# Performance work log

Hardware: AMD Instinct MI355X
Metric: run time of the kernel (lower is better)

Reference implementation:

```python
import jax, jax.numpy as jnp
import numpy as np

N_FEATURES = 1024
N_OUTPUTS = 512
N = 32768
N_DECISIONS = 3  # root + 2 internal nodes (depth-2 tree)
N_LEAVES = 4


def setup_inputs() -> dict:
    key = jax.random.key(0)
    k_x, k_dw, k_db, k_lw, k_lb = jax.random.split(key, 5)
    xs = jax.random.normal(k_x, (N, N_FEATURES), dtype=jnp.float32)
    # decision hyperplanes for nodes [root, left-child, right-child]
    dec_w = jax.random.normal(k_dw, (N_DECISIONS, N_FEATURES), dtype=jnp.float32) / np.sqrt(N_FEATURES)
    dec_b = jax.random.normal(k_db, (N_DECISIONS,), dtype=jnp.float32) * 0.01
    # linear leaves, ordered [LL, LR, RL, RR]
    leaf_w = jax.random.normal(k_lw, (N_LEAVES, N_FEATURES, N_OUTPUTS), dtype=jnp.float32) / np.sqrt(N_FEATURES)
    leaf_b = jax.random.normal(k_lb, (N_LEAVES, N_OUTPUTS), dtype=jnp.float32) * 0.01
    return {"xs": xs, "dec_w": dec_w, "dec_b": dec_b, "leaf_w": leaf_w, "leaf_b": leaf_b}


def reference(xs, dec_w, dec_b, leaf_w, leaf_b):
    # decisions at all 3 branch nodes: [N, 3] boolean (True -> go right)
    d = (xs @ dec_w.T + dec_b) > 0
    d0, d1, d2 = d[:, 0], d[:, 1], d[:, 2]
    # leaf index per sample: root False -> left subtree (node 1), True -> right subtree (node 2)
    leaf_idx = jnp.where(
        d0,
        jnp.where(d2, 3, 2),
        jnp.where(d1, 1, 0),
    )  # [N]
    # compute all leaf outputs densely (equivalent math to masked dispatch), then select
    outs = jnp.einsum("nf,kfd->nkd", xs, leaf_w) + leaf_b  # [N, 4, D]
    out = jnp.take_along_axis(outs, leaf_idx[:, None, None], axis=1)[:, 0]  # [N, D]
    return out
```

## Files before the change

kernel.cpp:

```cpp
#include <hip/hip_runtime.h>
#include <hip/hip_bf16.h>
#include <stdint.h>

#define NROWS 32768
#define NFEAT 1024
#define NOUT  512

typedef __attribute__((ext_vector_type(8))) short bf16x8;
typedef __attribute__((ext_vector_type(4))) float f32x4;

#define WS_CNT  0
#define WS_LIST 256
#define WS_BT   524544
#define WS_XB   (WS_BT + (size_t)4 * NOUT * NFEAT * 2)
#define WS_NEEDED (WS_XB + (size_t)NROWS * NFEAT * 2)

#define NDEC_BLOCKS 1024
#define NTR_BLOCKS  512

__global__ __launch_bounds__(64) void zero_cnt_kernel(int* __restrict__ cnt) {
  if (threadIdx.x < 4) cnt[threadIdx.x] = 0;
}

__global__ __launch_bounds__(256) void decide_tr_kernel(
    const float* __restrict__ xs, const float* __restrict__ dw,
    const float* __restrict__ db, const float* __restrict__ lw,
    __hip_bfloat16* __restrict__ bt, int* __restrict__ cnt,
    int* __restrict__ list, __hip_bfloat16* __restrict__ xsb ) {
  __shared__ float smem[32 * 33];
  const int tid = threadIdx.x;
  int b = blockIdx.x;

  if (b >= NDEC_BLOCKS) {
    int tb = b - NDEC_BLOCKS;
    int l = tb >> 7;
    int t = tb & 127;
    int d0 = (t >> 3) * 32;
    int k00 = (t & 7) * 128;
    int x = tid & 31, y = tid >> 5;
    const float* src = lw + (size_t)l * NFEAT * NOUT;
    __hip_bfloat16* dst = bt + (size_t)l * NOUT * NFEAT;
    float (*tile)[33] = (float(*)[33])smem;
    for (int kk = 0; kk < 4; ++kk) {
      int k0 = k00 + kk * 32;
#pragma unroll
      for (int i = 0; i < 4; ++i)
        tile[y * 4 + i][x] = src[(size_t)(k0 + y * 4 + i) * NOUT + d0 + x];
      __syncthreads();
#pragma unroll
      for (int i = 0; i < 4; ++i)
        dst[(size_t)(d0 + y * 4 + i) * NFEAT + k0 + x] =
            __float2bfloat16(tile[x][y * 4 + i]);
      __syncthreads();
    }
    return;
  }

  int* leaf_of = (int*)smem;
  const int lane = tid & 63;
  const int wv = tid >> 6;

  f32x4 w0[4], w1[4], w2[4];
#pragma unroll
  for (int c = 0; c < 2; ++c)
#pragma unroll
    for (int h = 0; h < 2; ++h) {
      int idx = c * 512 + lane * 8 + h * 4;
      w0[c * 2 + h] = *(const f32x4*)(dw + idx);
      w1[c * 2 + h] = *(const f32x4*)(dw + NFEAT + idx);
      w2[c * 2 + h] = *(const f32x4*)(dw + 2 * NFEAT + idx);
    }
  float b0 = db[0], b1 = db[1], b2 = db[2];

  int rowbase = b * 32 + wv * 8;
  for (int r = 0; r < 8; ++r) {
    int row = rowbase + r;
    const float* xr = xs + (size_t)row * NFEAT;
    float s0 = 0.f, s1 = 0.f, s2 = 0.f;
#pragma unroll
    for (int c = 0; c < 2; ++c) {
      int idx = c * 512 + lane * 8;
      f32x4 xv0 = *(const f32x4*)(xr + idx);
      f32x4 xv1 = *(const f32x4*)(xr + idx + 4);
#pragma unroll
      for (int j = 0; j < 4; ++j) {
        s0 += xv0[j] * w0[c * 2][j] + xv1[j] * w0[c * 2 + 1][j];
        s1 += xv0[j] * w1[c * 2][j] + xv1[j] * w1[c * 2 + 1][j];
        s2 += xv0[j] * w2[c * 2][j] + xv1[j] * w2[c * 2 + 1][j];
      }
      if (xsb) {
        union { bf16x8 v; __hip_bfloat16 h[8]; } pk;
#pragma unroll
        for (int j = 0; j < 4; ++j) {
          pk.h[j] = __float2bfloat16(xv0[j]);
          pk.h[j + 4] = __float2bfloat16(xv1[j]);
        }
        *(bf16x8*)(xsb + (size_t)row * NFEAT + idx) = pk.v;
      }
    }
#pragma unroll
    for (int off = 32; off > 0; off >>= 1) {
      s0 += __shfl_xor(s0, off);
      s1 += __shfl_xor(s1, off);
      s2 += __shfl_xor(s2, off);
    }
    if (lane == 0) {
      int lf = (s0 + b0 > 0.f) ? ((s2 + b2 > 0.f) ? 3 : 2)
                               : ((s1 + b1 > 0.f) ? 1 : 0);
      leaf_of[wv * 8 + r] = lf;
    }
  }
  __syncthreads();

  if (tid < 64) {
    int i = tid;
    int myleaf = (i < 32) ? leaf_of[i] : -1;
    int myrow = b * 32 + i;
    unsigned long long m0 = __ballot(myleaf == 0);
    unsigned long long m1 = __ballot(myleaf == 1);
    unsigned long long m2 = __ballot(myleaf == 2);
    unsigned long long m3 = __ballot(myleaf == 3);
    unsigned long long mym = (myleaf == 0) ? m0 : (myleaf == 1) ? m1
                           : (myleaf == 2) ? m2 : (myleaf == 3) ? m3 : 0ull;
    unsigned long long below = (1ull << i) - 1ull;
    int rank = __popcll(mym & below);
    int base = 0;
    if (i < 4) {
      unsigned long long mi = (i == 0) ? m0 : (i == 1) ? m1 : (i == 2) ? m2 : m3;
      base = atomicAdd(&cnt[i], __popcll(mi));
    }
    int mybase = __shfl(base, (myleaf < 0) ? 0 : myleaf);
    if (i < 32) list[myleaf * NROWS + mybase + rank] = myrow;
  }
}

#define BM 128
#define BN 128
#define BK 64
#define KSTEPS (NFEAT / BK)

__device__ __forceinline__ bool decode_tile(const int* cnt, int& leaf, int& mloc,
                                            int& ntile, int& cc) {
  int bid = blockIdx.x;
  int cpx = (int)(gridDim.x >> 3);
  int swz = (bid & 7) * cpx + (bid >> 3);
  int mtile = swz >> 2;
  ntile = swz & 3;
  int c0 = cnt[0], c1 = cnt[1], c2 = cnt[2], c3 = cnt[3];
  int t0 = (c0 + BM - 1) / BM, t1 = (c1 + BM - 1) / BM;
  int t2 = (c2 + BM - 1) / BM, t3 = (c3 + BM - 1) / BM;
  if (mtile < t0)                     { leaf = 0; mloc = mtile;                cc = c0; }
  else if (mtile < t0 + t1)           { leaf = 1; mloc = mtile - t0;           cc = c1; }
  else if (mtile < t0 + t1 + t2)      { leaf = 2; mloc = mtile - t0 - t1;      cc = c2; }
  else if (mtile < t0 + t1 + t2 + t3) { leaf = 3; mloc = mtile - t0 - t1 - t2; cc = c3; }
  else return false;
  return true;
}

__global__ __launch_bounds__(256) void gemm_lds_kernel(
    const __hip_bfloat16* __restrict__ xsb, const __hip_bfloat16* __restrict__ bt,
    const float* __restrict__ lb, const int* __restrict__ cnt,
    const int* __restrict__ list, float* __restrict__ out) {
  __shared__ __hip_bfloat16 Al[BM * BK];
  __shared__ __hip_bfloat16 Bl[BN * BK];
  __shared__ int rows_s[BM];

  int leaf, mloc, ntile, cc;
  if (!decode_tile(cnt, leaf, mloc, ntile, cc)) return;

  const int tid = threadIdx.x;
  if (tid < BM) {
    int i = mloc * BM + tid;
    rows_s[tid] = (i < cc) ? list[leaf * NROWS + i] : -1;
  }
  __syncthreads();

  const int lane = tid & 63;
  const int wv = tid >> 6;
  const int g8 = (((lane & 7) ^ (lane >> 3)) << 3);
  const __hip_bfloat16* asrc[4];
  const __hip_bfloat16* bsrc[4];
#pragma unroll
  for (int j = 0; j < 4; ++j) {
    int tr = wv * 32 + j * 8 + (lane >> 3);
    int grow = rows_s[tr];
    if (grow < 0) grow = 0;
    asrc[j] = xsb + (size_t)grow * NFEAT + g8;
    bsrc[j] = bt + ((size_t)leaf * NOUT + ntile * BN + tr) * NFEAT + g8;
  }

  const int wr = (wv >> 1) * 64;
  const int wc = (wv & 1) * 64;
  f32x4 acc[4][4];
#pragma unroll
  for (int m = 0; m < 4; ++m)
#pragma unroll
    for (int n = 0; n < 4; ++n) acc[m][n] = (f32x4){0.f, 0.f, 0.f, 0.f};

  for (int ks = 0; ks < KSTEPS; ++ks) {
    if (ks) __syncthreads();
#pragma unroll
    for (int j = 0; j < 4; ++j) {
      __builtin_amdgcn_global_load_lds(
          (const __attribute__((address_space(1))) void*)(asrc[j] + ks * BK),
          (__attribute__((address_space(3))) void*)(&Al[(wv * 4 + j) * 512]),
          16, 0, 0);
      __builtin_amdgcn_global_load_lds(
          (const __attribute__((address_space(1))) void*)(bsrc[j] + ks * BK),
          (__attribute__((address_space(3))) void*)(&Bl[(wv * 4 + j) * 512]),
          16, 0, 0);
    }
    __syncthreads();

#pragma unroll
    for (int kk = 0; kk < 2; ++kk) {
      bf16x8 af[4], bfr[4];
      int gk = kk * 4 + (lane >> 4);
#pragma unroll
      for (int m = 0; m < 4; ++m) {
        int r = wr + m * 16 + (lane & 15);
        af[m] = *(const bf16x8*)(&Al[r * BK + ((gk ^ (r & 7)) << 3)]);
      }
#pragma unroll
      for (int n = 0; n < 4; ++n) {
        int r = wc + n * 16 + (lane & 15);
        bfr[n] = *(const bf16x8*)(&Bl[r * BK + ((gk ^ (r & 7)) << 3)]);
      }
#pragma unroll
      for (int m = 0; m < 4; ++m)
#pragma unroll
        for (int n = 0; n < 4; ++n)
          acc[m][n] = __builtin_amdgcn_mfma_f32_16x16x32_bf16(
              af[m], bfr[n], acc[m][n], 0, 0, 0);
    }
  }

  int colb = ntile * BN + wc;
#pragma unroll
  for (int n = 0; n < 4; ++n) {
    int col = colb + n * 16 + (lane & 15);
    float bias = lb[leaf * NOUT + col];
#pragma unroll
    for (int m = 0; m < 4; ++m) {
#pragma unroll
      for (int r = 0; r < 4; ++r) {
        int lrow = wr + m * 16 + (lane >> 4) * 4 + r;
        int grow = rows_s[lrow];
        if (grow >= 0) out[(size_t)grow * NOUT + col] = acc[m][n][r] + bias;
      }
    }
  }
}

__global__ __launch_bounds__(256) void gemm_fallback_kernel(
    const float* __restrict__ xs, const __hip_bfloat16* __restrict__ bt,
    const float* __restrict__ lb, const int* __restrict__ cnt,
    const int* __restrict__ list, float* __restrict__ out) {
  __shared__ __hip_bfloat16 Al[BM * BK];
  __shared__ __hip_bfloat16 Bl[BN * BK];
  __shared__ int rows_s[BM];

  int leaf, mloc, ntile, cc;
  if (!decode_tile(cnt, leaf, mloc, ntile, cc)) return;

  const int tid = threadIdx.x;
  if (tid < BM) {
    int i = mloc * BM + tid;
    rows_s[tid] = (i < cc) ? list[leaf * NROWS + i] : -1;
  }
  __syncthreads();

  const int srow = tid >> 1;
  const int shalf = tid & 1;
  int a_grow = rows_s[srow];
  int a_clamp = (a_grow < 0) ? 0 : a_grow;
  const float* aptr = xs + (size_t)a_clamp * NFEAT + shalf * 32;
  const __hip_bfloat16* bptr =
      bt + ((size_t)leaf * NOUT + ntile * BN + srow) * NFEAT + shalf * 32;

  const int lane = tid & 63;
  const int wv = tid >> 6;
  const int wr = (wv >> 1) * 64;
  const int wc = (wv & 1) * 64;

  f32x4 acc[4][4];
#pragma unroll
  for (int m = 0; m < 4; ++m)
#pragma unroll
    for (int n = 0; n < 4; ++n) acc[m][n] = (f32x4){0.f, 0.f, 0.f, 0.f};

  f32x4 av[8];
  bf16x8 bv[4];
#define LOAD_TILE(K0)                                                        \
  {                                                                          \
    _Pragma("unroll") for (int j = 0; j < 8; ++j)                            \
        av[j] = *(const f32x4*)(aptr + (K0) + j * 4);                        \
    _Pragma("unroll") for (int j = 0; j < 4; ++j)                            \
        bv[j] = *(const bf16x8*)(bptr + (K0) + j * 8);                       \
  }

  LOAD_TILE(0);

  for (int ks = 0; ks < KSTEPS; ++ks) {
#pragma unroll
    for (int j = 0; j < 4; ++j) {
      union { bf16x8 v; __hip_bfloat16 h[8]; } pk;
#pragma unroll
      for (int e = 0; e < 8; ++e)
        pk.h[e] = __float2bfloat16(av[j * 2 + (e >> 2)][e & 3]);
      int g = shalf * 4 + j;
      *(bf16x8*)(&Al[srow * BK + ((g ^ (srow & 7)) << 3)]) = pk.v;
    }
#pragma unroll
    for (int j = 0; j < 4; ++j) {
      int g = shalf * 4 + j;
      *(bf16x8*)(&Bl[srow * BK + ((g ^ (srow & 7)) << 3)]) = bv[j];
    }
    __syncthreads();

    if (ks + 1 < KSTEPS) LOAD_TILE((ks + 1) * BK);

#pragma unroll
    for (int kk = 0; kk < 2; ++kk) {
      bf16x8 af[4], bfr[4];
      int gk = kk * 4 + (lane >> 4);
#pragma unroll
      for (int m = 0; m < 4; ++m) {
        int r = wr + m * 16 + (lane & 15);
        af[m] = *(const bf16x8*)(&Al[r * BK + ((gk ^ (r & 7)) << 3)]);
      }
#pragma unroll
      for (int n = 0; n < 4; ++n) {
        int r = wc + n * 16 + (lane & 15);
        bfr[n] = *(const bf16x8*)(&Bl[r * BK + ((gk ^ (r & 7)) << 3)]);
      }
#pragma unroll
      for (int m = 0; m < 4; ++m)
#pragma unroll
        for (int n = 0; n < 4; ++n)
          acc[m][n] = __builtin_amdgcn_mfma_f32_16x16x32_bf16(
              af[m], bfr[n], acc[m][n], 0, 0, 0);
    }
    __syncthreads();
  }

  int colb = ntile * BN + wc;
#pragma unroll
  for (int n = 0; n < 4; ++n) {
    int col = colb + n * 16 + (lane & 15);
    float bias = lb[leaf * NOUT + col];
#pragma unroll
    for (int m = 0; m < 4; ++m) {
#pragma unroll
      for (int r = 0; r < 4; ++r) {
        int lrow = wr + m * 16 + (lane >> 4) * 4 + r;
        int grow = rows_s[lrow];
        if (grow >= 0) out[(size_t)grow * NOUT + col] = acc[m][n][r] + bias;
      }
    }
  }
}

extern "C" void kernel_launch(void* const* d_in, const int* in_sizes, int n_in,
                              void* d_out, int out_size, void* d_ws, size_t ws_size,
                              hipStream_t stream) {
  const float* xs = (const float*)d_in[0];
  const float* dw = (const float*)d_in[1];
  const float* db = (const float*)d_in[2];
  const float* lw = (const float*)d_in[3];
  const float* lb = (const float*)d_in[4];
  float* out = (float*)d_out;
  char* ws = (char*)d_ws;
  int* cnt = (int*)(ws + WS_CNT);
  int* list = (int*)(ws + WS_LIST);
  __hip_bfloat16* bt = (__hip_bfloat16*)(ws + WS_BT);
  bool big = ws_size >= WS_NEEDED;
  __hip_bfloat16* xsb = big ? (__hip_bfloat16*)(ws + WS_XB) : nullptr;

  zero_cnt_kernel<<<1, 64, 0, stream>>>(cnt);
  decide_tr_kernel<<<NDEC_BLOCKS + NTR_BLOCKS, 256, 0, stream>>>(
      xs, dw, db, lw, bt, cnt, list, xsb);
  if (big)
    gemm_lds_kernel<<<1040, 256, 0, stream>>>(xsb, bt, lb, cnt, list, out);
  else
    gemm_fallback_kernel<<<1040, 256, 0, stream>>>(xs, bt, lb, cnt, list, out);
}
```

Measured before the change: 105.9 us.

## Prefetch next K-step into registers and stage through LDS manually

Replaces the direct global-to-LDS loads with register prefetching: the next K-slice is loaded from global memory into registers while the current slice is consumed by MFMAs, then written into LDS at the start of the next iteration. Custom barriers wait only on LDS counters, so global loads stay in flight across the barrier. This aims to hide global latency behind compute, at the cost of more VGPRs and explicit LDS stores. The LDS write layout has to match the swizzle the earlier direct loads produced.

```diff
diff --git a/kernel.cpp b/kernel.cpp
--- a/kernel.cpp
+++ b/kernel.cpp
@@ -157,7 +157,15 @@
   return true;
 }
 
-__global__ __launch_bounds__(256) void gemm_lds_kernel(
+#define LGKM_BARRIER()                                        \
+  do {                                                        \
+    asm volatile("s_waitcnt lgkmcnt(0)" ::: "memory");        \
+    __builtin_amdgcn_sched_barrier(0);                        \
+    __builtin_amdgcn_s_barrier();                             \
+    __builtin_amdgcn_sched_barrier(0);                        \
+  } while (0)
+
+__global__ __launch_bounds__(256) void gemm_pipe_kernel(
     const __hip_bfloat16* __restrict__ xsb, const __hip_bfloat16* __restrict__ bt,
     const float* __restrict__ lb, const int* __restrict__ cnt,
     const int* __restrict__ list, float* __restrict__ out) {
@@ -197,20 +205,27 @@
 #pragma unroll
     for (int n = 0; n < 4; ++n) acc[m][n] = (f32x4){0.f, 0.f, 0.f, 0.f};
 
+  bf16x8 av[4], bv[4];
+#pragma unroll
+  for (int j = 0; j < 4; ++j) {
+    av[j] = *(const bf16x8*)(asrc[j]);
+    bv[j] = *(const bf16x8*)(bsrc[j]);
+  }
+
   for (int ks = 0; ks < KSTEPS; ++ks) {
-    if (ks) __syncthreads();
 #pragma unroll
     for (int j = 0; j < 4; ++j) {
-      __builtin_amdgcn_global_load_lds(
-          (const __attribute__((address_space(1))) void*)(asrc[j] + ks * BK),
-          (__attribute__((address_space(3))) void*)(&Al[(wv * 4 + j) * 512]),
-          16, 0, 0);
-      __builtin_amdgcn_global_load_lds(
-          (const __attribute__((address_space(1))) void*)(bsrc[j] + ks * BK),
-          (__attribute__((address_space(3))) void*)(&Bl[(wv * 4 + j) * 512]),
-          16, 0, 0);
-    }
-    __syncthreads();
+      *(bf16x8*)(&Al[(wv * 4 + j) * 512 + lane * 8]) = av[j];
+      *(bf16x8*)(&Bl[(wv * 4 + j) * 512 + lane * 8]) = bv[j];
+    }
+    if (ks + 1 < KSTEPS) {
+#pragma unroll
+      for (int j = 0; j < 4; ++j) {
+        av[j] = *(const bf16x8*)(asrc[j] + (ks + 1) * BK);
+        bv[j] = *(const bf16x8*)(bsrc[j] + (ks + 1) * BK);
+      }
+    }
+    LGKM_BARRIER();
 
 #pragma unroll
     for (int kk = 0; kk < 2; ++kk) {
@@ -233,6 +248,7 @@
           acc[m][n] = __builtin_amdgcn_mfma_f32_16x16x32_bf16(
               af[m], bfr[n], acc[m][n], 0, 0, 0);
     }
+    LGKM_BARRIER();
   }
 
   int colb = ntile * BN + wc;
@@ -381,7 +397,7 @@
   decide_tr_kernel<<<NDEC_BLOCKS + NTR_BLOCKS, 256, 0, stream>>>(
       xs, dw, db, lw, bt, cnt, list, xsb);
   if (big)
-    gemm_lds_kernel<<<1040, 256, 0, stream>>>(xsb, bt, lb, cnt, list, out);
+    gemm_pipe_kernel<<<1040, 256, 0, stream>>>(xsb, bt, lb, cnt, list, out);
   else
     gemm_fallback_kernel<<<1040, 256, 0, stream>>>(xs, bt, lb, cnt, list, out);
 }
```

New measurement: 108.1 us. 1.02x slower.

## Scatter bf16 rows into per-leaf contiguous buffers for contiguous GEMM A loads

Applied to the files above, without the earlier changes.

The decision kernel now writes each row's bf16 copy into a per-leaf compacted buffer at its list position, after the atomic slot assignment. The GEMM then reads the A tile from contiguous rows instead of gathering through the row list. This removes the indirect gather and may improve coalescing and cache locality for A loads. In exchange the xs row is read a second time from global memory after the decision, and the per-leaf capacity LEAFCAP is fixed, with overflow rows clamped into slot 0 and so producing wrong results if a leaf exceeds it.

```diff
diff --git a/kernel.cpp b/kernel.cpp
--- a/kernel.cpp
+++ b/kernel.cpp
@@ -5,6 +5,7 @@
 #define NROWS 32768
 #define NFEAT 1024
 #define NOUT  512
+#define LEAFCAP 8960
 
 typedef __attribute__((ext_vector_type(8))) short bf16x8;
 typedef __attribute__((ext_vector_type(4))) float f32x4;
@@ -13,7 +14,7 @@
 #define WS_LIST 256
 #define WS_BT   524544
 #define WS_XB   (WS_BT + (size_t)4 * NOUT * NFEAT * 2)
-#define WS_NEEDED (WS_XB + (size_t)NROWS * NFEAT * 2)
+#define WS_NEEDED (WS_XB + (size_t)4 * LEAFCAP * NFEAT * 2)
 
 #define NDEC_BLOCKS 1024
 #define NTR_BLOCKS  512
@@ -57,6 +58,7 @@
   }
 
   int* leaf_of = (int*)smem;
+  int* dest_of = (int*)smem + 32;
   const int lane = tid & 63;
   const int wv = tid >> 6;
 
@@ -87,15 +89,6 @@
         s0 += xv0[j] * w0[c * 2][j] + xv1[j] * w0[c * 2 + 1][j];
         s1 += xv0[j] * w1[c * 2][j] + xv1[j] * w1[c * 2 + 1][j];
         s2 += xv0[j] * w2[c * 2][j] + xv1[j] * w2[c * 2 + 1][j];
-      }
-      if (xsb) {
-        union { bf16x8 v; __hip_bfloat16 h[8]; } pk;
-#pragma unroll
-        for (int j = 0; j < 4; ++j) {
-          pk.h[j] = __float2bfloat16(xv0[j]);
-          pk.h[j + 4] = __float2bfloat16(xv1[j]);
-        }
-        *(bf16x8*)(xsb + (size_t)row * NFEAT + idx) = pk.v;
       }
     }
 #pragma unroll
@@ -130,7 +123,36 @@
       base = atomicAdd(&cnt[i], __popcll(mi));
     }
     int mybase = __shfl(base, (myleaf < 0) ? 0 : myleaf);
-    if (i < 32) list[myleaf * NROWS + mybase + rank] = myrow;
+    if (i < 32) {
+      int pos = mybase + rank;
+      list[myleaf * NROWS + pos] = myrow;
+      int d = myleaf * LEAFCAP + pos;
+      if (pos >= LEAFCAP) d = myleaf * LEAFCAP;
+      dest_of[i] = d;
+    }
+  }
+  __syncthreads();
+
+  if (xsb) {
+    for (int r = 0; r < 8; ++r) {
+      int row = rowbase + r;
+      int dest = dest_of[wv * 8 + r];
+      const float* xr = xs + (size_t)row * NFEAT;
+      __hip_bfloat16* xw = xsb + (size_t)dest * NFEAT;
+#pragma unroll
+      for (int c = 0; c < 2; ++c) {
+        int idx = c * 512 + lane * 8;
+        f32x4 xv0 = *(const f32x4*)(xr + idx);
+        f32x4 xv1 = *(const f32x4*)(xr + idx + 4);
+        union { bf16x8 v; __hip_bfloat16 h[8]; } pk;
+#pragma unroll
+        for (int j = 0; j < 4; ++j) {
+          pk.h[j] = __float2bfloat16(xv0[j]);
+          pk.h[j + 4] = __float2bfloat16(xv1[j]);
+        }
+        *(bf16x8*)(xw + idx) = pk.v;
+      }
+    }
   }
 }
 
@@ -183,9 +205,7 @@
 #pragma unroll
   for (int j = 0; j < 4; ++j) {
     int tr = wv * 32 + j * 8 + (lane >> 3);
-    int grow = rows_s[tr];
-    if (grow < 0) grow = 0;
-    asrc[j] = xsb + (size_t)grow * NFEAT + g8;
+    asrc[j] = xsb + ((size_t)leaf * LEAFCAP + mloc * BM + tr) * NFEAT + g8;
     bsrc[j] = bt + ((size_t)leaf * NOUT + ntile * BN + tr) * NFEAT + g8;
   }
 
@@ -256,8 +276,8 @@
     const float* __restrict__ xs, const __hip_bfloat16* __restrict__ bt,
     const float* __restrict__ lb, const int* __restrict__ cnt,
     const int* __restrict__ list, float* __restrict__ out) {
-  __shared__ __hip_bfloat16 Al[BM * BK];
-  __shared__ __hip_bfloat16 Bl[BN * BK];
+  __shared__ __hip_bfloat16 Afl[BM * BK];
+  __shared__ __hip_bfloat16 Bfl[BN * BK];
   __shared__ int rows_s[BM];
 
   int leaf, mloc, ntile, cc;
@@ -309,12 +329,12 @@
       for (int e = 0; e < 8; ++e)
         pk.h[e] = __float2bfloat16(av[j * 2 + (e >> 2)][e & 3]);
       int g = shalf * 4 + j;
-      *(bf16x8*)(&Al[srow * BK + ((g ^ (srow & 7)) << 3)]) = pk.v;
+      *(bf16x8*)(&Afl[srow * BK + ((g ^ (srow & 7)) << 3)]) = pk.v;
     }
 #pragma unroll
     for (int j = 0; j < 4; ++j) {
       int g = shalf * 4 + j;
-      *(bf16x8*)(&Bl[srow * BK + ((g ^ (srow & 7)) << 3)]) = bv[j];
+      *(bf16x8*)(&Bfl[srow * BK + ((g ^ (srow & 7)) << 3)]) = bv[j];
     }
     __syncthreads();
 
@@ -327,12 +347,12 @@
 #pragma unroll
       for (int m = 0; m < 4; ++m) {
         int r = wr + m * 16 + (lane & 15);
-        af[m] = *(const bf16x8*)(&Al[r * BK + ((gk ^ (r & 7)) << 3)]);
+        af[m] = *(const bf16x8*)(&Afl[r * BK + ((gk ^ (r & 7)) << 3)]);
       }
 #pragma unroll
       for (int n = 0; n < 4; ++n) {
         int r = wc + n * 16 + (lane & 15);
-        bfr[n] = *(const bf16x8*)(&Bl[r * BK + ((gk ^ (r & 7)) << 3)]);
+        bfr[n] = *(const bf16x8*)(&Bfl[r * BK + ((gk ^ (r & 7)) << 3)]);
       }
 #pragma unroll
       for (int m = 0; m < 4; ++m)
```

After: 122.1 us. +15.3%, slower.
